# Kernel optimization log

Hardware: AMD Instinct MI355X
Metric: run time of the kernel (lower is better)

## Reference

```python
import jax, jax.numpy as jnp
import numpy as np
from jax import lax

TRAJ_STEPS = 50  # output_dim=100 -> 50 (x,y) waypoints


def setup_inputs() -> dict:
    key = jax.random.key(0)
    ks = jax.random.split(key, 12)
    s = 0.05  # small init scale to keep gates out of saturation
    return {
        "x": jax.random.normal(ks[0], (32768, 256), jnp.float32),
        "W1": jax.random.normal(ks[1], (256, 64), jnp.float32) * s,
        "b1": jax.random.normal(ks[2], (64,), jnp.float32) * s,
        "W2": jax.random.normal(ks[3], (64, 64), jnp.float32) * s,
        "b2": jax.random.normal(ks[4], (64,), jnp.float32) * s,
        "Wih": jax.random.normal(ks[5], (2, 192), jnp.float32) * s,   # GRU input weights, gate order (r,z,n)
        "bih": jax.random.normal(ks[6], (192,), jnp.float32) * s,
        "Whh": jax.random.normal(ks[7], (64, 192), jnp.float32) * s,  # GRU hidden weights
        "bhh": jax.random.normal(ks[8], (192,), jnp.float32) * s,
        "Wout": jax.random.normal(ks[9], (64, 2), jnp.float32) * s,
        "bout": jax.random.normal(ks[10], (2,), jnp.float32) * s,
    }


def _forward(x, W1, b1, W2, b2, Wih, bih, Whh, bhh, Wout, bout):
    H = W2.shape[1]
    # backbone MLP -> initial hidden state
    z = jax.nn.relu(x @ W1 + b1)
    z = jax.nn.relu(z @ W2 + b2)  # [B, H]

    def step(carry, _):
        wp, h = carry                      # wp: [B,2] current waypoint, h: [B,H]
        gi = wp @ Wih + bih                # [B, 3H]
        gh = h @ Whh + bhh                 # [B, 3H]
        ir, iz, inn = gi[..., :H], gi[..., H:2 * H], gi[..., 2 * H:]
        hr, hz, hn = gh[..., :H], gh[..., H:2 * H], gh[..., 2 * H:]
        r = jax.nn.sigmoid(ir + hr)
        u = jax.nn.sigmoid(iz + hz)
        n = jnp.tanh(inn + r * hn)
        h_new = (1.0 - u) * n + u * h      # PyTorch GRUCell update
        dx = jax.nn.sigmoid(h_new @ Wout + bout)  # [B,2]
        wp_new = wp + dx                   # residual accumulation
        return (wp_new, h_new), wp_new

    wp0 = jnp.zeros(x.shape[:-1] + (2,), z.dtype)
    _, wps = lax.scan(step, (wp0, z), None, length=TRAJ_STEPS)  # [T, B, 2]
    wps = jnp.moveaxis(wps, 0, -2)                              # [B, T, 2]
    return wps.reshape(x.shape[:-1] + (2 * TRAJ_STEPS,))        # [B, 2T]


def reference(x, W1, b1, W2, b2, Wih, bih, Whh, bhh, Wout, bout):
    return _forward(x, W1, b1, W2, b2, Wih, bih, Whh, bhh, Wout, bout)
```

## Files before the change

kernel.cpp:

```cpp
#include <hip/hip_runtime.h>
#include <hip/hip_bf16.h>

#define TRAJ 50

typedef __attribute__((ext_vector_type(8))) short short8;
typedef __attribute__((ext_vector_type(4))) float f32x4;
typedef __attribute__((ext_vector_type(2))) float f32x2;

#if defined(__has_builtin)
#if __has_builtin(__builtin_amdgcn_exp2f)
#define EXP2F(x) __builtin_amdgcn_exp2f(x)
#else
#define EXP2F(x) exp2f(x)
#endif
#if __has_builtin(__builtin_amdgcn_rcpf)
#define RCPF(x) __builtin_amdgcn_rcpf(x)
#else
#define RCPF(x) (1.0f/(x))
#endif
#else
#define EXP2F(x) exp2f(x)
#define RCPF(x) (1.0f/(x))
#endif

#define BAR() asm volatile("s_waitcnt lgkmcnt(0)\n\ts_barrier" ::: "memory")

__device__ __forceinline__ unsigned short f2bf(float f){
  union { float f; unsigned u; } v; v.f = f;
  unsigned u = v.u;
  u += 0x7FFFu + ((u >> 16) & 1u);
  return (unsigned short)(u >> 16);
}
__device__ __forceinline__ unsigned pk(unsigned short a, unsigned short b){
  return (unsigned)a | ((unsigned)b << 16);
}
__device__ __forceinline__ unsigned pkbf(float a, float b){
  union { __hip_bfloat162 h; unsigned u; } c;
  c.h = __float22bfloat162_rn(make_float2(a, b));
  return c.u;
}
__device__ __forceinline__ short8 mkfrag(uint2 v){
  union { unsigned u[4]; short8 s; } c;
  c.u[0] = v.x; c.u[1] = v.y; c.u[2] = 0u; c.u[3] = 0u;
  return c.s;
}

#define MFMA16(A,B,C) __builtin_amdgcn_mfma_f32_16x16x32_bf16((A),(B),(C),0,0,0)

#define SSC (-1.44269504f)
#define TSC ( 2.88539008f)

__device__ __forceinline__ f32x2 exp2v(f32x2 v){ return (f32x2){EXP2F(v[0]), EXP2F(v[1])}; }
__device__ __forceinline__ f32x2 rcpv (f32x2 v){ return (f32x2){RCPF(v[0]), RCPF(v[1])}; }

__device__ __forceinline__ f32x2 gru_pair(f32x2 r_, f32x2 u_, f32x2 n_, f32x2 i_, f32x2 hp){
  const f32x2 one = (f32x2){1.f, 1.f};
  f32x2 d1 = exp2v(r_) + one;
  f32x2 d2 = exp2v(u_) + one;
  f32x2 rp = rcpv(d1 * d2);
  f32x2 rv = d2 * rp;
  f32x2 uv = d1 * rp;
  f32x2 y  = __builtin_elementwise_fma(rv, n_, i_);
  f32x2 nv = one - 2.f * rcpv(exp2v(y) + one);
  return __builtin_elementwise_fma(uv, hp - nv, nv);
}

__global__ __launch_bounds__(512, 4) void gru_actor_kernel(
    const float* __restrict__ x,
    const float* __restrict__ W1, const float* __restrict__ b1,
    const float* __restrict__ W2, const float* __restrict__ b2,
    const float* __restrict__ Wih, const float* __restrict__ bih,
    const float* __restrict__ Whh, const float* __restrict__ bhh,
    const float* __restrict__ Wout, const float* __restrict__ bout,
    float* __restrict__ out)
{
  __shared__ __align__(16) char sm_x[32768];
  __shared__ __align__(16) char sm_w[32768];
  __shared__ __align__(16) char sm_w2[8192];
  __shared__ float sm_b1[64];
  __shared__ float sm_b2[64];

  const int t    = threadIdx.x;
  const int row0 = blockIdx.x * 64;
  const int w    = t >> 6;
  const int pair = w >> 1;
  const int p    = w & 1;
  const int l    = t & 63;
  const int lr   = l & 15;
  const int lg   = l >> 4;
  const int myrow = pair * 16 + lr;
  const int swz  = (lr & 7) << 4;

  {
    const float4* xg = (const float4*)(x + (size_t)row0 * 256);
    #pragma unroll
    for (int it = 0; it < 8; ++it){
      int fi = t + it * 512;
      float4 v = xg[fi];
      int e = fi * 4, row = e >> 8, col = e & 255;
      *(uint2*)(sm_x + row * 512 + ((col * 2) ^ ((row & 7) << 4))) =
          make_uint2(pkbf(v.x, v.y), pkbf(v.z, v.w));
    }
  }
  for (int n = t; n < 16384; n += 512){
    int i = n & 63, kk = n >> 6;
    *(unsigned short*)(sm_w + i * 512 + ((kk * 2) ^ ((i & 7) << 4))) = f2bf(W1[kk * 64 + i]);
  }
  for (int n = t; n < 4096; n += 512){
    int i = n & 63, kk = n >> 6;
    *(unsigned short*)(sm_w2 + i * 128 + ((kk * 2) ^ ((i & 7) << 4))) = f2bf(W2[kk * 64 + i]);
  }
  if (t < 64){ sm_b1[t] = b1[t]; sm_b2[t] = b2[t]; }
  __syncthreads();

  const int ar0 = 16 * (2 * p + 0) + lr;
  const int ar1 = 16 * (2 * p + 1) + lr;
  f32x4 accL0, accL1;
  {
    float4 bva = *(const float4*)(sm_b1 + 16 * (2 * p + 0) + lg * 4);
    float4 bvb = *(const float4*)(sm_b1 + 16 * (2 * p + 1) + lg * 4);
    accL0 = (f32x4){bva.x, bva.y, bva.z, bva.w};
    accL1 = (f32x4){bvb.x, bvb.y, bvb.z, bvb.w};
  }
  #pragma unroll
  for (int kb = 0; kb < 8; ++kb){
    short8 B  = *(const short8*)(sm_x + myrow * 512 + ((kb * 64 + lg * 16) ^ swz));
    short8 Aa = *(const short8*)(sm_w + ar0 * 512 + ((kb * 64 + lg * 16) ^ swz));
    short8 Ab = *(const short8*)(sm_w + ar1 * 512 + ((kb * 64 + lg * 16) ^ swz));
    accL0 = MFMA16(Aa, B, accL0);
    accL1 = MFMA16(Ab, B, accL1);
  }
  __syncthreads();

  {
    f32x4 a0 = accL0, a1 = accL1;
    *(uint2*)(sm_x + myrow * 128 + ((64 * p + 0  + 8 * lg) ^ swz)) =
        make_uint2(pkbf(fmaxf(a0[0],0.f), fmaxf(a0[1],0.f)), pkbf(fmaxf(a0[2],0.f), fmaxf(a0[3],0.f)));
    *(uint2*)(sm_x + myrow * 128 + ((64 * p + 32 + 8 * lg) ^ swz)) =
        make_uint2(pkbf(fmaxf(a1[0],0.f), fmaxf(a1[1],0.f)), pkbf(fmaxf(a1[2],0.f), fmaxf(a1[3],0.f)));
  }
  for (int n = t; n < 12288; n += 512){
    int kk = n / 192, i = n - kk * 192;
    float s = (i < 128) ? SSC : TSC;
    *(unsigned short*)(sm_w + i * 128 + ((kk * 2) ^ ((i & 7) << 4))) = f2bf(s * Whh[kk * 192 + i]);
  }
  __syncthreads();

  f32x2 h2[4];
  {
    f32x4 acc20, acc21;
    float4 bva = *(const float4*)(sm_b2 + 16 * (2 * p + 0) + lg * 4);
    float4 bvb = *(const float4*)(sm_b2 + 16 * (2 * p + 1) + lg * 4);
    acc20 = (f32x4){bva.x, bva.y, bva.z, bva.w};
    acc21 = (f32x4){bvb.x, bvb.y, bvb.z, bvb.w};
    #pragma unroll
    for (int kb = 0; kb < 2; ++kb){
      short8 B  = *(const short8*)(sm_x + myrow * 128 + ((kb * 64 + lg * 16) ^ swz));
      short8 Aa = *(const short8*)(sm_w2 + ar0 * 128 + ((kb * 64 + lg * 16) ^ swz));
      short8 Ab = *(const short8*)(sm_w2 + ar1 * 128 + ((kb * 64 + lg * 16) ^ swz));
      acc20 = MFMA16(Aa, B, acc20);
      acc21 = MFMA16(Ab, B, acc21);
    }
    h2[0] = (f32x2){fmaxf(acc20[0],0.f), fmaxf(acc20[1],0.f)};
    h2[1] = (f32x2){fmaxf(acc20[2],0.f), fmaxf(acc20[3],0.f)};
    h2[2] = (f32x2){fmaxf(acc21[0],0.f), fmaxf(acc21[1],0.f)};
    h2[3] = (f32x2){fmaxf(acc21[2],0.f), fmaxf(acc21[3],0.f)};
    *(uint2*)(sm_x + 8192 + myrow * 128 + ((64 * p + 0  + 8 * lg) ^ swz)) =
        make_uint2(pkbf(h2[0][0], h2[0][1]), pkbf(h2[1][0], h2[1][1]));
    *(uint2*)(sm_x + 8192 + myrow * 128 + ((64 * p + 32 + 8 * lg) ^ swz)) =
        make_uint2(pkbf(h2[2][0], h2[2][1]), pkbf(h2[3][0], h2[3][1]));
  }

  short8 Ah[3][2][2];
  #pragma unroll
  for (int g = 0; g < 3; ++g){
    #pragma unroll
    for (int tql = 0; tql < 2; ++tql){
      int i = g * 64 + 32 * p + 16 * tql + lr;
      #pragma unroll
      for (int kb = 0; kb < 2; ++kb)
        Ah[g][tql][kb] = *(const short8*)(sm_w + i * 128 + ((kb * 64 + lg * 16) ^ swz));
    }
  }
  uint2 Ak2p[4][2] = {};
  if (lg == 0){
    #pragma unroll
    for (int tql = 0; tql < 2; ++tql){
      int dr = 32 * p + 16 * tql + lr;
      int du = 64 + dr, dn = 128 + dr;
      Ak2p[0][tql] = make_uint2(pk(f2bf(SSC*Wih[dr]), f2bf(SSC*Wih[192+dr])),
                                pk(f2bf(SSC*(bih[dr]+bhh[dr])), 0));
      Ak2p[1][tql] = make_uint2(pk(f2bf(SSC*Wih[du]), f2bf(SSC*Wih[192+du])),
                                pk(f2bf(SSC*(bih[du]+bhh[du])), 0));
      Ak2p[2][tql] = make_uint2(0u, pk(f2bf(TSC*bhh[dn]), 0));
      Ak2p[3][tql] = make_uint2(pk(f2bf(TSC*Wih[dn]), f2bf(TSC*Wih[192+dn])),
                                pk(f2bf(TSC*bih[dn]), 0));
    }
  }
  short8 AoR[2];
  #pragma unroll
  for (int kb = 0; kb < 2; ++kb){
    short8 f = (short8){0,0,0,0,0,0,0,0};
    if (lr < 2){
      #pragma unroll
      for (int j = 0; j < 8; ++j){
        int k = kb * 32 + lg * 8 + j;
        f[j] = (short)f2bf(SSC * Wout[k * 2 + lr]);
      }
    }
    AoR[kb] = f;
  }
  const float bo0 = SSC * bout[0], bo1 = SSC * bout[1];
  __syncthreads();

  float wp0 = 0.f, wp1 = 0.f;
  float* outp = out + (size_t)(row0 + myrow) * 100;
  short8 B0 = *(const short8*)(sm_x + 8192 + myrow * 128 + ((0  + lg * 16) ^ swz));
  short8 B1 = *(const short8*)(sm_x + 8192 + myrow * 128 + ((64 + lg * 16) ^ swz));

  #pragma unroll 2
  for (int s = 0; s < TRAJ; ++s){
    char* bufW = sm_x + ((s & 1) << 13);
    short8 B2;
    {
      unsigned b2lo = 0u, b2hi = 0u;
      if (lg == 0){ b2lo = pkbf(wp0, wp1); b2hi = 0x00003F80u; }
      union { unsigned u[4]; short8 sv; } c;
      c.u[0] = b2lo; c.u[1] = b2hi; c.u[2] = 0u; c.u[3] = 0u;
      B2 = c.sv;
    }
    #pragma unroll
    for (int tql = 0; tql < 2; ++tql){
      f32x4 aR = (f32x4){0,0,0,0}, aU = (f32x4){0,0,0,0};
      f32x4 aN = (f32x4){0,0,0,0}, aI = (f32x4){0,0,0,0};
      aR = MFMA16(Ah[0][tql][0], B0, aR);
      aR = MFMA16(Ah[0][tql][1], B1, aR);
      aR = MFMA16(mkfrag(Ak2p[0][tql]), B2, aR);
      aU = MFMA16(Ah[1][tql][0], B0, aU);
      aU = MFMA16(Ah[1][tql][1], B1, aU);
      aU = MFMA16(mkfrag(Ak2p[1][tql]), B2, aU);
      aN = MFMA16(Ah[2][tql][0], B0, aN);
      aN = MFMA16(Ah[2][tql][1], B1, aN);
      aN = MFMA16(mkfrag(Ak2p[2][tql]), B2, aN);
      aI = MFMA16(mkfrag(Ak2p[3][tql]), B2, aI);
      f32x2 hA = gru_pair((f32x2){aR[0],aR[1]}, (f32x2){aU[0],aU[1]},
                          (f32x2){aN[0],aN[1]}, (f32x2){aI[0],aI[1]}, h2[2*tql+0]);
      f32x2 hB = gru_pair((f32x2){aR[2],aR[3]}, (f32x2){aU[2],aU[3]},
                          (f32x2){aN[2],aN[3]}, (f32x2){aI[2],aI[3]}, h2[2*tql+1]);
      h2[2*tql+0] = hA; h2[2*tql+1] = hB;
      *(uint2*)(bufW + myrow * 128 + ((64 * p + 32 * tql + 8 * lg) ^ swz)) =
          make_uint2(pkbf(hA[0], hA[1]), pkbf(hB[0], hB[1]));
    }
    BAR();
    short8 nB0 = *(const short8*)(bufW + myrow * 128 + ((0  + lg * 16) ^ swz));
    short8 nB1 = *(const short8*)(bufW + myrow * 128 + ((64 + lg * 16) ^ swz));
    f32x4 aD = (f32x4){0,0,0,0};
    if (lg == 0){ aD[0] = bo0; aD[1] = bo1; }
    aD = MFMA16(AoR[0], nB0, aD);
    aD = MFMA16(AoR[1], nB1, aD);
    if (lg == 0){
      float ea = EXP2F(aD[0]), eb = EXP2F(aD[1]);
      float da = 1.f + ea, db = 1.f + eb;
      float rp = RCPF(da * db);
      wp0 += db * rp;
      wp1 += da * rp;
      if (p == 0) *(float2*)(outp + 2 * s) = make_float2(wp0, wp1);
    }
    B0 = nB0; B1 = nB1;
  }
}

extern "C" void kernel_launch(void* const* d_in, const int* in_sizes, int n_in,
                              void* d_out, int out_size, void* d_ws, size_t ws_size,
                              hipStream_t stream) {
  (void)n_in; (void)out_size; (void)d_ws; (void)ws_size;
  const float* x    = (const float*)d_in[0];
  const float* W1   = (const float*)d_in[1];
  const float* b1   = (const float*)d_in[2];
  const float* W2   = (const float*)d_in[3];
  const float* b2   = (const float*)d_in[4];
  const float* Wih  = (const float*)d_in[5];
  const float* bih  = (const float*)d_in[6];
  const float* Whh  = (const float*)d_in[7];
  const float* bhh  = (const float*)d_in[8];
  const float* Wout = (const float*)d_in[9];
  const float* bout = (const float*)d_in[10];
  float* out = (float*)d_out;

  int nrows = in_sizes[0] / 256;
  int grid  = nrows / 64;
  gru_actor_kernel<<<dim3(grid), dim3(512), 0, stream>>>(
      x, W1, b1, W2, b2, Wih, bih, Whh, bhh, Wout, bout, out);
}
```

Measured before the change: 118.9 us.

## Shrink blocks to 16 rows and gather weights from global into registers

Result: slower. 131.7 us (+10.8%).

```diff
diff --git a/kernel.cpp b/kernel.cpp
--- a/kernel.cpp
+++ b/kernel.cpp
@@ -65,7 +65,20 @@
   return __builtin_elementwise_fma(uv, hp - nv, nv);
 }
 
-__global__ __launch_bounds__(512, 4) void gru_actor_kernel(
+__device__ __forceinline__ short8 gatherA(const float* __restrict__ M, int N,
+                                          int k0, int i, float scale){
+  const float* q = M + (size_t)k0 * N + i;
+  union { unsigned u[4]; short8 s; } c;
+  #pragma unroll
+  for (int j = 0; j < 4; ++j){
+    float a = q[(2*j  ) * N];
+    float b = q[(2*j+1) * N];
+    c.u[j] = pk(f2bf(scale * a), f2bf(scale * b));
+  }
+  return c.s;
+}
+
+__global__ __launch_bounds__(128, 3) void gru_actor_kernel(
     const float* __restrict__ x,
     const float* __restrict__ W1, const float* __restrict__ b1,
     const float* __restrict__ W2, const float* __restrict__ b2,
@@ -74,112 +87,85 @@
     const float* __restrict__ Wout, const float* __restrict__ bout,
     float* __restrict__ out)
 {
-  __shared__ __align__(16) char sm_x[32768];
-  __shared__ __align__(16) char sm_w[32768];
-  __shared__ __align__(16) char sm_w2[8192];
-  __shared__ float sm_b1[64];
-  __shared__ float sm_b2[64];
+  __shared__ __align__(16) char sm_h[4096];
 
   const int t    = threadIdx.x;
-  const int row0 = blockIdx.x * 64;
-  const int w    = t >> 6;
-  const int pair = w >> 1;
-  const int p    = w & 1;
+  const int p    = t >> 6;
   const int l    = t & 63;
   const int lr   = l & 15;
   const int lg   = l >> 4;
-  const int myrow = pair * 16 + lr;
+  const int rowbase = blockIdx.x * 16;
   const int swz  = (lr & 7) << 4;
 
+  f32x4 accL[2];
+  #pragma unroll
+  for (int tql = 0; tql < 2; ++tql){
+    float4 bv = *(const float4*)(b1 + 16 * (2*p + tql) + 4 * lg);
+    accL[tql] = (f32x4){bv.x, bv.y, bv.z, bv.w};
+  }
   {
-    const float4* xg = (const float4*)(x + (size_t)row0 * 256);
-    #pragma unroll
-    for (int it = 0; it < 8; ++it){
-      int fi = t + it * 512;
-      float4 v = xg[fi];
-      int e = fi * 4, row = e >> 8, col = e & 255;
-      *(uint2*)(sm_x + row * 512 + ((col * 2) ^ ((row & 7) << 4))) =
-          make_uint2(pkbf(v.x, v.y), pkbf(v.z, v.w));
-    }
-  }
-  for (int n = t; n < 16384; n += 512){
-    int i = n & 63, kk = n >> 6;
-    *(unsigned short*)(sm_w + i * 512 + ((kk * 2) ^ ((i & 7) << 4))) = f2bf(W1[kk * 64 + i]);
-  }
-  for (int n = t; n < 4096; n += 512){
-    int i = n & 63, kk = n >> 6;
-    *(unsigned short*)(sm_w2 + i * 128 + ((kk * 2) ^ ((i & 7) << 4))) = f2bf(W2[kk * 64 + i]);
-  }
-  if (t < 64){ sm_b1[t] = b1[t]; sm_b2[t] = b2[t]; }
-  __syncthreads();
-
-  const int ar0 = 16 * (2 * p + 0) + lr;
-  const int ar1 = 16 * (2 * p + 1) + lr;
-  f32x4 accL0, accL1;
-  {
-    float4 bva = *(const float4*)(sm_b1 + 16 * (2 * p + 0) + lg * 4);
-    float4 bvb = *(const float4*)(sm_b1 + 16 * (2 * p + 1) + lg * 4);
-    accL0 = (f32x4){bva.x, bva.y, bva.z, bva.w};
-    accL1 = (f32x4){bvb.x, bvb.y, bvb.z, bvb.w};
-  }
-  #pragma unroll
-  for (int kb = 0; kb < 8; ++kb){
-    short8 B  = *(const short8*)(sm_x + myrow * 512 + ((kb * 64 + lg * 16) ^ swz));
-    short8 Aa = *(const short8*)(sm_w + ar0 * 512 + ((kb * 64 + lg * 16) ^ swz));
-    short8 Ab = *(const short8*)(sm_w + ar1 * 512 + ((kb * 64 + lg * 16) ^ swz));
-    accL0 = MFMA16(Aa, B, accL0);
-    accL1 = MFMA16(Ab, B, accL1);
-  }
-  __syncthreads();
-
-  {
-    f32x4 a0 = accL0, a1 = accL1;
-    *(uint2*)(sm_x + myrow * 128 + ((64 * p + 0  + 8 * lg) ^ swz)) =
+    const float* xrow = x + (size_t)(rowbase + lr) * 256;
+    #pragma unroll
+    for (int kb = 0; kb < 8; ++kb){
+      int k0 = kb * 32 + lg * 8;
+      float4 xa = *(const float4*)(xrow + k0);
+      float4 xb = *(const float4*)(xrow + k0 + 4);
+      union { unsigned u[4]; short8 s; } bc;
+      bc.u[0] = pkbf(xa.x, xa.y); bc.u[1] = pkbf(xa.z, xa.w);
+      bc.u[2] = pkbf(xb.x, xb.y); bc.u[3] = pkbf(xb.z, xb.w);
+      #pragma unroll
+      for (int tql = 0; tql < 2; ++tql){
+        short8 A = gatherA(W1, 64, k0, 16 * (2*p + tql) + lr, 1.0f);
+        accL[tql] = MFMA16(A, bc.s, accL[tql]);
+      }
+    }
+  }
+  #pragma unroll
+  for (int tql = 0; tql < 2; ++tql){
+    f32x4 a0 = accL[tql];
+    *(uint2*)(sm_h + lr * 128 + ((64 * p + 32 * tql + 8 * lg) ^ swz)) =
         make_uint2(pkbf(fmaxf(a0[0],0.f), fmaxf(a0[1],0.f)), pkbf(fmaxf(a0[2],0.f), fmaxf(a0[3],0.f)));
-    *(uint2*)(sm_x + myrow * 128 + ((64 * p + 32 + 8 * lg) ^ swz)) =
-        make_uint2(pkbf(fmaxf(a1[0],0.f), fmaxf(a1[1],0.f)), pkbf(fmaxf(a1[2],0.f), fmaxf(a1[3],0.f)));
-  }
-  for (int n = t; n < 12288; n += 512){
-    int kk = n / 192, i = n - kk * 192;
-    float s = (i < 128) ? SSC : TSC;
-    *(unsigned short*)(sm_w + i * 128 + ((kk * 2) ^ ((i & 7) << 4))) = f2bf(s * Whh[kk * 192 + i]);
   }
   __syncthreads();
 
   f32x2 h2[4];
   {
-    f32x4 acc20, acc21;
-    float4 bva = *(const float4*)(sm_b2 + 16 * (2 * p + 0) + lg * 4);
-    float4 bvb = *(const float4*)(sm_b2 + 16 * (2 * p + 1) + lg * 4);
-    acc20 = (f32x4){bva.x, bva.y, bva.z, bva.w};
-    acc21 = (f32x4){bvb.x, bvb.y, bvb.z, bvb.w};
+    f32x4 acc2[2];
+    #pragma unroll
+    for (int tql = 0; tql < 2; ++tql){
+      float4 bv = *(const float4*)(b2 + 16 * (2*p + tql) + 4 * lg);
+      acc2[tql] = (f32x4){bv.x, bv.y, bv.z, bv.w};
+    }
     #pragma unroll
     for (int kb = 0; kb < 2; ++kb){
-      short8 B  = *(const short8*)(sm_x + myrow * 128 + ((kb * 64 + lg * 16) ^ swz));
-      short8 Aa = *(const short8*)(sm_w2 + ar0 * 128 + ((kb * 64 + lg * 16) ^ swz));
-      short8 Ab = *(const short8*)(sm_w2 + ar1 * 128 + ((kb * 64 + lg * 16) ^ swz));
-      acc20 = MFMA16(Aa, B, acc20);
-      acc21 = MFMA16(Ab, B, acc21);
-    }
-    h2[0] = (f32x2){fmaxf(acc20[0],0.f), fmaxf(acc20[1],0.f)};
-    h2[1] = (f32x2){fmaxf(acc20[2],0.f), fmaxf(acc20[3],0.f)};
-    h2[2] = (f32x2){fmaxf(acc21[0],0.f), fmaxf(acc21[1],0.f)};
-    h2[3] = (f32x2){fmaxf(acc21[2],0.f), fmaxf(acc21[3],0.f)};
-    *(uint2*)(sm_x + 8192 + myrow * 128 + ((64 * p + 0  + 8 * lg) ^ swz)) =
+      short8 B = *(const short8*)(sm_h + lr * 128 + ((kb * 64 + lg * 16) ^ swz));
+      #pragma unroll
+      for (int tql = 0; tql < 2; ++tql){
+        short8 A = gatherA(W2, 64, kb * 32 + lg * 8, 16 * (2*p + tql) + lr, 1.0f);
+        acc2[tql] = MFMA16(A, B, acc2[tql]);
+      }
+    }
+    h2[0] = (f32x2){fmaxf(acc2[0][0],0.f), fmaxf(acc2[0][1],0.f)};
+    h2[1] = (f32x2){fmaxf(acc2[0][2],0.f), fmaxf(acc2[0][3],0.f)};
+    h2[2] = (f32x2){fmaxf(acc2[1][0],0.f), fmaxf(acc2[1][1],0.f)};
+    h2[3] = (f32x2){fmaxf(acc2[1][2],0.f), fmaxf(acc2[1][3],0.f)};
+    __syncthreads();
+    *(uint2*)(sm_h + 2048 + lr * 128 + ((64 * p + 0  + 8 * lg) ^ swz)) =
         make_uint2(pkbf(h2[0][0], h2[0][1]), pkbf(h2[1][0], h2[1][1]));
-    *(uint2*)(sm_x + 8192 + myrow * 128 + ((64 * p + 32 + 8 * lg) ^ swz)) =
+    *(uint2*)(sm_h + 2048 + lr * 128 + ((64 * p + 32 + 8 * lg) ^ swz)) =
         make_uint2(pkbf(h2[2][0], h2[2][1]), pkbf(h2[3][0], h2[3][1]));
   }
 
   short8 Ah[3][2][2];
   #pragma unroll
   for (int g = 0; g < 3; ++g){
+    float s = (g < 2) ? SSC : TSC;
     #pragma unroll
     for (int tql = 0; tql < 2; ++tql){
       int i = g * 64 + 32 * p + 16 * tql + lr;
       #pragma unroll
       for (int kb = 0; kb < 2; ++kb)
-        Ah[g][tql][kb] = *(const short8*)(sm_w + i * 128 + ((kb * 64 + lg * 16) ^ swz));
+        Ah[g][tql][kb] = gatherA(Whh, 192, kb * 32 + lg * 8, i, s);
     }
   }
   uint2 Ak2p[4][2] = {};
@@ -214,13 +200,13 @@
   __syncthreads();
 
   float wp0 = 0.f, wp1 = 0.f;
-  float* outp = out + (size_t)(row0 + myrow) * 100;
-  short8 B0 = *(const short8*)(sm_x + 8192 + myrow * 128 + ((0  + lg * 16) ^ swz));
-  short8 B1 = *(const short8*)(sm_x + 8192 + myrow * 128 + ((64 + lg * 16) ^ swz));
+  float* outp = out + (size_t)(rowbase + lr) * 100;
+  short8 B0 = *(const short8*)(sm_h + 2048 + lr * 128 + ((0  + lg * 16) ^ swz));
+  short8 B1 = *(const short8*)(sm_h + 2048 + lr * 128 + ((64 + lg * 16) ^ swz));
 
   #pragma unroll 2
   for (int s = 0; s < TRAJ; ++s){
-    char* bufW = sm_x + ((s & 1) << 13);
+    char* bufW = sm_h + ((s & 1) << 11);
     short8 B2;
     {
       unsigned b2lo = 0u, b2hi = 0u;
@@ -248,12 +234,12 @@
       f32x2 hB = gru_pair((f32x2){aR[2],aR[3]}, (f32x2){aU[2],aU[3]},
                           (f32x2){aN[2],aN[3]}, (f32x2){aI[2],aI[3]}, h2[2*tql+1]);
       h2[2*tql+0] = hA; h2[2*tql+1] = hB;
-      *(uint2*)(bufW + myrow * 128 + ((64 * p + 32 * tql + 8 * lg) ^ swz)) =
+      *(uint2*)(bufW + lr * 128 + ((64 * p + 32 * tql + 8 * lg) ^ swz)) =
           make_uint2(pkbf(hA[0], hA[1]), pkbf(hB[0], hB[1]));
     }
     BAR();
-    short8 nB0 = *(const short8*)(bufW + myrow * 128 + ((0  + lg * 16) ^ swz));
-    short8 nB1 = *(const short8*)(bufW + myrow * 128 + ((64 + lg * 16) ^ swz));
+    short8 nB0 = *(const short8*)(bufW + lr * 128 + ((0  + lg * 16) ^ swz));
+    short8 nB1 = *(const short8*)(bufW + lr * 128 + ((64 + lg * 16) ^ swz));
     f32x4 aD = (f32x4){0,0,0,0};
     if (lg == 0){ aD[0] = bo0; aD[1] = bo1; }
     aD = MFMA16(AoR[0], nB0, aD);
@@ -288,7 +274,7 @@
   float* out = (float*)d_out;
 
   int nrows = in_sizes[0] / 256;
-  int grid  = nrows / 64;
-  gru_actor_kernel<<<dim3(grid), dim3(512), 0, stream>>>(
+  int grid  = nrows / 16;
+  gru_actor_kernel<<<dim3(grid), dim3(128), 0, stream>>>(
       x, W1, b1, W2, b2, Wih, bih, Whh, bhh, Wout, bout, out);
 }
```
